# Kernel optimization log

Hardware: AMD Instinct MI355X
Metric: run time of the kernel (lower is better)

## Reference

```python
import jax, jax.numpy as jnp
import numpy as np

N_NODES = 50000
N_EDGES = 1_600_000
D_NODE = 64
D_EDGE = 16
HEADS = 4
ATT_F = 16  # features[0] / heads = 64 / 4
LN_EPS = 1e-6


def setup_inputs() -> dict:
    key = jax.random.key(0)
    ks = jax.random.split(key, 9)
    nodes = jax.random.normal(ks[0], (N_NODES, D_NODE), dtype=jnp.float32)
    edges = jax.random.normal(ks[1], (N_EDGES, D_EDGE), dtype=jnp.float32)
    receivers = jax.random.randint(ks[2], (N_EDGES,), 0, N_NODES)
    senders = jax.random.randint(ks[3], (N_EDGES,), 0, N_NODES)
    # he_normal-like scale for W (fan_in = input feature dim)
    W = jax.random.normal(ks[4], (HEADS, ATT_F, D_NODE), dtype=jnp.float32) * np.sqrt(2.0 / D_NODE)
    W_edge = jax.random.normal(ks[5], (HEADS, ATT_F, D_EDGE), dtype=jnp.float32) * np.sqrt(2.0 / D_EDGE)
    # xavier_normal-like scale for a
    a = jax.random.normal(ks[6], (HEADS, 3 * ATT_F), dtype=jnp.float32) * np.sqrt(2.0 / (HEADS + 3 * ATT_F))
    ln_scale = jnp.ones((HEADS * ATT_F,), dtype=jnp.float32)
    ln_bias = jnp.zeros((HEADS * ATT_F,), dtype=jnp.float32)
    return {"nodes": nodes, "edges": edges, "receivers": receivers, "senders": senders,
            "W": W, "W_edge": W_edge, "a": a, "ln_scale": ln_scale, "ln_bias": ln_bias}


def reference(nodes, edges, receivers, senders, W, W_edge, a, ln_scale, ln_bias):
    n = nodes.shape[0]
    # add self edges (zero edge features)
    self_idx = jnp.arange(n)
    r = jnp.concatenate([receivers, self_idx], axis=0)          # [Etot]
    s = jnp.concatenate([senders, self_idx], axis=0)            # [Etot]
    e = jnp.concatenate([edges, jnp.zeros((n, edges.shape[1]), edges.dtype)], axis=0)  # [Etot, De]

    # project node features once, then gather per edge
    Wn = jnp.einsum('hfi,ni->nhf', W, nodes)                    # [N, H, F]
    Ws = Wn[s]                                                   # [Etot, H, F]
    Wr = Wn[r]                                                   # [Etot, H, F]
    We = jnp.einsum('hfi,ei->ehf', W_edge, e)                   # [Etot, H, F]

    # attention logits: a . [Ws || Wr || We], computed without materializing the concat
    a_s, a_r, a_e = jnp.split(a, 3, axis=-1)                    # each [H, F]
    msg = (jnp.einsum('ehf,hf->eh', Ws, a_s)
           + jnp.einsum('ehf,hf->eh', Wr, a_r)
           + jnp.einsum('ehf,hf->eh', We, a_e))                 # [Etot, H]
    lm = jax.nn.leaky_relu(msg)

    # segment softmax over edges grouped by receiver
    seg_max = jax.ops.segment_max(lm, r, num_segments=n)        # [N, H]
    z = lm - seg_max[r]
    exp_z = jnp.exp(z)
    norm = jax.ops.segment_sum(exp_z, r, num_segments=n)        # [N, H]
    alpha = exp_z / norm[r]                                     # [Etot, H]

    # attention-weighted scatter-sum aggregation
    att_msg = alpha[:, :, None] * Ws                            # [Etot, H, F]
    aggr = jax.ops.segment_sum(att_msg, r, num_segments=n)      # [N, H, F]
    out = aggr.reshape(n, -1)                                   # [N, H*F]

    out = jax.nn.elu(out)
    # LayerNorm (flax default: eps=1e-6, scale & bias over last axis)
    mean = jnp.mean(out, axis=-1, keepdims=True)
    var = jnp.mean(jnp.square(out - mean), axis=-1, keepdims=True)
    out = (out - mean) * jax.lax.rsqrt(var + LN_EPS)
    out = out * ln_scale + ln_bias
    return out
```

## Files before the change

kernel.cpp:

```cpp
#include <hip/hip_runtime.h>
#include <hip/hip_fp16.h>

#define LEAKY_SLOPE 0.01f
#define LN_EPS 1e-6f
#define SUBS 8
#define CAP 352
#define MAXE (SUBS*CAP)
#define CSTRIDE 16

__device__ __forceinline__ float head_sel(int h, float a, float b, float c, float d) {
    float lo = (h & 1) ? b : a;
    float hi = (h & 1) ? d : c;
    return (h & 2) ? hi : lo;
}

__device__ __forceinline__ int xcc_id() {
    return (int)(__builtin_amdgcn_s_getreg(20 | (3 << 11)) & 7);
}

__global__ __launch_bounds__(256) void node_proj_kernel(
    const float* __restrict__ nodes, const float* __restrict__ W,
    const float* __restrict__ a, float* __restrict__ Wn,
    float* __restrict__ s_s, float* __restrict__ s_r,
    float* __restrict__ lm_self, int N)
{
    __shared__ float Wt[64][65];
    int t = threadIdx.x;
    #pragma unroll
    for (int k = 0; k < 16; k++) {
        int flat = k * 256 + t;
        Wt[flat & 63][flat >> 6] = W[flat];
    }
    __syncthreads();
    int lane = t & 63;
    int n = blockIdx.x * 4 + (t >> 6);
    if (n >= N) return;
    float nv = nodes[(size_t)n * 64 + lane];
    float acc = 0.f;
    #pragma unroll
    for (int i = 0; i < 64; i++)
        acc += Wt[i][lane] * __shfl(nv, i);
    Wn[(size_t)n * 64 + lane] = acc;
    int h = lane >> 4, f = lane & 15;
    float ps = acc * a[h * 48 + f];
    float pr = acc * a[h * 48 + 16 + f];
    #pragma unroll
    for (int off = 1; off < 16; off <<= 1) {
        ps += __shfl_xor(ps, off);
        pr += __shfl_xor(pr, off);
    }
    if (f == 0) {
        s_s[n * 4 + h] = ps;
        s_r[n * 4 + h] = pr;
        float v = ps + pr;
        lm_self[n * 4 + h] = v > 0.f ? v : LEAKY_SLOPE * v;
    }
}

__global__ __launch_bounds__(256) void edge_bin_kernel(
    const float* __restrict__ edges, const int* __restrict__ receivers,
    const int* __restrict__ senders, const float* __restrict__ W_edge,
    const float* __restrict__ a, const float* __restrict__ s_s,
    const float* __restrict__ s_r, int* __restrict__ cursor,
    int4* __restrict__ slab, int E)
{
    __shared__ float be[4][16];
    int t = threadIdx.x;
    int e = blockIdx.x * 256 + t;
    bool act = e < E;
    int r = 0, s = 0;
    if (act) { r = receivers[e]; s = senders[e]; }
    if (t < 64) {
        int h = t >> 4, i = t & 15;
        float sm = 0.f;
        #pragma unroll
        for (int f = 0; f < 16; f++)
            sm += W_edge[(h * 16 + f) * 16 + i] * a[h * 48 + 32 + f];
        be[h][i] = sm;
    }
    __syncthreads();
    if (!act) return;

    int b = r >> 6;
    int cidx = b * SUBS + xcc_id();
    int slot = atomicAdd(&cursor[cidx * CSTRIDE], 1);

    const float4* ef = (const float4*)(edges + (size_t)e * 16);
    float4 e0 = ef[0], e1 = ef[1], e2 = ef[2], e3 = ef[3];
    float4 ssv = ((const float4*)s_s)[s];
    float4 srv = ((const float4*)s_r)[r];
    float ev[16] = {e0.x, e0.y, e0.z, e0.w, e1.x, e1.y, e1.z, e1.w,
                    e2.x, e2.y, e2.z, e2.w, e3.x, e3.y, e3.z, e3.w};
    float ssa[4] = {ssv.x, ssv.y, ssv.z, ssv.w};
    float sra[4] = {srv.x, srv.y, srv.z, srv.w};
    float lm[4];
    #pragma unroll
    for (int hh = 0; hh < 4; hh++) {
        float se = 0.f;
        #pragma unroll
        for (int i = 0; i < 16; i++) se += be[hh][i] * ev[i];
        float v = ssa[hh] + sra[hh] + se;
        lm[hh] = v > 0.f ? v : LEAKY_SLOPE * v;
    }
    if (slot < CAP) {
        unsigned packA = (unsigned)__half_as_ushort(__float2half(lm[2])) |
                         ((unsigned)__half_as_ushort(__float2half(lm[3])) << 16);
        unsigned packB = (unsigned)s | ((unsigned)(r & 63) << 16);
        slab[(size_t)cidx * CAP + slot] =
            make_int4(__float_as_int(lm[0]), __float_as_int(lm[1]),
                      (int)packA, (int)packB);
    }
}

__global__ __launch_bounds__(256) void bucket_sort_kernel(
    const int* __restrict__ cursor, int4* __restrict__ slab,
    int2* __restrict__ meta, int N)
{
    __shared__ int4 raw[MAXE];
    __shared__ unsigned short perm[MAXE];
    __shared__ int cnt64[64];
    __shared__ int off64[64];
    __shared__ int cur64[64];

    int b = blockIdx.x;
    int t = threadIdx.x;
    int nn = min(64, N - b * 64);

    if (t < 64) cnt64[t] = 0;
    __syncthreads();

    int c[SUBS], basearr[SUBS];
    int tot = 0;
    #pragma unroll
    for (int sub = 0; sub < SUBS; sub++) {
        int cc = min(cursor[(b * SUBS + sub) * CSTRIDE], CAP);
        c[sub] = cc; basearr[sub] = tot; tot += cc;
    }

    #pragma unroll
    for (int sub = 0; sub < SUBS; sub++) {
        int cc = c[sub], bs = basearr[sub];
        const int4* src = slab + (size_t)(b * SUBS + sub) * CAP;
        for (int i = t; i < cc; i += 256) {
            int4 p = src[i];
            raw[bs + i] = p;
            atomicAdd(&cnt64[((unsigned)p.w >> 16) & 63], 1);
        }
    }
    __syncthreads();

    if (t < 64) {
        int v = cnt64[t];
        int incl = v;
        #pragma unroll
        for (int off = 1; off < 64; off <<= 1) {
            int u = __shfl_up(incl, off);
            if (t >= off) incl += u;
        }
        off64[t] = incl - v;
        cur64[t] = incl - v;
    }
    __syncthreads();

    for (int i = t; i < tot; i += 256) {
        int rl = ((unsigned)raw[i].w >> 16) & 63;
        int pos = atomicAdd(&cur64[rl], 1);
        perm[pos] = (unsigned short)i;
    }
    __syncthreads();

    int4* dst = slab + (size_t)b * MAXE;
    for (int pos = t; pos < tot; pos += 256)
        dst[pos] = raw[perm[pos]];

    if (t < nn)
        meta[b * 64 + t] = make_int2(b * MAXE + off64[t], cnt64[t]);
}

__global__ __launch_bounds__(256) void node_aggr_kernel(
    const float* __restrict__ Wn, const float* __restrict__ lm_self,
    const int2* __restrict__ meta, const int4* __restrict__ sorted,
    const float* __restrict__ ln_scale, const float* __restrict__ ln_bias,
    float* __restrict__ out, int N)
{
    __shared__ float lds_w[4][64][4];
    __shared__ int   lds_s[4][64];
    int t = threadIdx.x;
    int lane = t & 63;
    int wv = t >> 6;
    int n = blockIdx.x * 4 + wv;
    if (n >= N) return;
    int2 mt = meta[n];
    int beg = mt.x, cntn = mt.y;
    int h = lane >> 4;

    float acc = 0.f, acc2 = 0.f;
    float p0 = 0.f, p1 = 0.f, p2 = 0.f, p3 = 0.f;

    for (int base = 0; base < cntn; base += 64) {
        int j = base + lane;
        float w0 = 0.f, w1 = 0.f, w2 = 0.f, w3 = 0.f;
        int sv = 0;
        if (j < cntn) {
            int4 pl = sorted[beg + j];
            w0 = __expf(__int_as_float(pl.x));
            w1 = __expf(__int_as_float(pl.y));
            unsigned pa = (unsigned)pl.z;
            w2 = __expf(__half2float(__ushort_as_half((unsigned short)(pa & 0xFFFFu))));
            w3 = __expf(__half2float(__ushort_as_half((unsigned short)(pa >> 16))));
            sv = (int)((unsigned)pl.w & 0xFFFFu);
        }
        p0 += w0; p1 += w1; p2 += w2; p3 += w3;
        lds_s[wv][lane] = sv;
        *(float4*)&lds_w[wv][lane][0] = make_float4(w0, w1, w2, w3);
        int cnt = min(64, cntn - base);
        int k = 0;
        for (; k + 1 < cnt; k += 2) {
            int   sk0 = lds_s[wv][k];
            int   sk1 = lds_s[wv][k + 1];
            float a0  = lds_w[wv][k][h];
            float a1  = lds_w[wv][k + 1][h];
            acc  += a0 * Wn[(size_t)sk0 * 64 + lane];
            acc2 += a1 * Wn[(size_t)sk1 * 64 + lane];
        }
        if (k < cnt)
            acc += lds_w[wv][k][h] * Wn[(size_t)lds_s[wv][k] * 64 + lane];
    }
    acc += acc2;

    #pragma unroll
    for (int off = 1; off < 64; off <<= 1) {
        p0 += __shfl_xor(p0, off);
        p1 += __shfl_xor(p1, off);
        p2 += __shfl_xor(p2, off);
        p3 += __shfl_xor(p3, off);
    }
    float4 ls = ((const float4*)lm_self)[n];
    float ws0 = __expf(ls.x), ws1 = __expf(ls.y);
    float ws2 = __expf(ls.z), ws3 = __expf(ls.w);
    float totd  = head_sel(h, p0 + ws0, p1 + ws1, p2 + ws2, p3 + ws3);
    float wself = head_sel(h, ws0, ws1, ws2, ws3);
    acc = (acc + wself * Wn[(size_t)n * 64 + lane]) / totd;

    float y = acc > 0.f ? acc : expm1f(acc);
    float sum = y;
    #pragma unroll
    for (int off = 1; off < 64; off <<= 1) sum += __shfl_xor(sum, off);
    float mean = sum * 0.015625f;
    float d = y - mean;
    float vs = d * d;
    #pragma unroll
    for (int off = 1; off < 64; off <<= 1) vs += __shfl_xor(vs, off);
    float var = vs * 0.015625f;
    float o = d * rsqrtf(var + LN_EPS) * ln_scale[lane] + ln_bias[lane];
    out[(size_t)n * 64 + lane] = o;
}

extern "C" void kernel_launch(void* const* d_in, const int* in_sizes, int n_in,
                              void* d_out, int out_size, void* d_ws, size_t ws_size,
                              hipStream_t stream) {
    const float* nodes     = (const float*)d_in[0];
    const float* edges     = (const float*)d_in[1];
    const int*   receivers = (const int*)d_in[2];
    const int*   senders   = (const int*)d_in[3];
    const float* W         = (const float*)d_in[4];
    const float* W_edge    = (const float*)d_in[5];
    const float* a         = (const float*)d_in[6];
    const float* ln_scale  = (const float*)d_in[7];
    const float* ln_bias   = (const float*)d_in[8];
    float* out = (float*)d_out;

    int N = in_sizes[0] / 64;
    int E = in_sizes[2];
    int NB = (N + 63) / 64;

    char* ws = (char*)d_ws;
    size_t off = 0;
    auto alloc = [&](size_t bytes) -> void* {
        void* p = ws + off;
        off += (bytes + 15) & ~(size_t)15;
        return p;
    };
    float* Wn      = (float*)alloc((size_t)N * 64 * 4);
    float* s_s     = (float*)alloc((size_t)N * 4 * 4);
    float* s_r     = (float*)alloc((size_t)N * 4 * 4);
    float* lm_self = (float*)alloc((size_t)N * 4 * 4);
    int*   cursor  = (int*)alloc((size_t)NB * SUBS * CSTRIDE * 4);
    int2*  meta    = (int2*)alloc((size_t)N * 8);
    int4*  slab    = (int4*)alloc((size_t)NB * MAXE * 16);
    (void)ws_size; (void)n_in; (void)out_size;

    hipMemsetAsync(cursor, 0, (size_t)NB * SUBS * CSTRIDE * 4, stream);

    node_proj_kernel<<<(N + 3) / 4, 256, 0, stream>>>(
        nodes, W, a, Wn, s_s, s_r, lm_self, N);
    edge_bin_kernel<<<(E + 255) / 256, 256, 0, stream>>>(
        edges, receivers, senders, W_edge, a, s_s, s_r, cursor, slab, E);
    bucket_sort_kernel<<<NB, 256, 0, stream>>>(cursor, slab, meta, N);
    node_aggr_kernel<<<(N + 3) / 4, 256, 0, stream>>>(
        Wn, lm_self, meta, slab, ln_scale, ln_bias, out, N);
}
```

Before: 375.3 us.

## Fuse bucket sort with per-node aggregation and drop the sorted slab write-back

The separate bucket-sort and aggregation kernels are merged into one kernel per 64-node bucket. The sort now builds only an LDS permutation of slab indices, and each wave then aggregates 16 nodes by reading slab entries through that permutation. This removes the sorted-slab write-back, the meta array and one kernel launch. The cursor atomic is also relaxed to workgroup scope to make binning cheaper. The cost is far fewer waves (one block per bucket, each wave handling nodes serially), which may hurt latency hiding on the gathers; the workgroup-scope atomic on a cross-block counter is also semantically risky.

```diff
diff --git a/kernel.cpp b/kernel.cpp
--- a/kernel.cpp
+++ b/kernel.cpp
@@ -16,6 +16,13 @@
 
 __device__ __forceinline__ int xcc_id() {
     return (int)(__builtin_amdgcn_s_getreg(20 | (3 << 11)) & 7);
+}
+
+__device__ __forceinline__ float unpack_lm(int h, int4 p) {
+    unsigned pa = (unsigned)p.z;
+    float lm2 = __half2float(__ushort_as_half((unsigned short)(pa & 0xFFFFu)));
+    float lm3 = __half2float(__ushort_as_half((unsigned short)(pa >> 16)));
+    return head_sel(h, __int_as_float(p.x), __int_as_float(p.y), lm2, lm3);
 }
 
 __global__ __launch_bounds__(256) void node_proj_kernel(
@@ -83,7 +90,9 @@
 
     int b = r >> 6;
     int cidx = b * SUBS + xcc_id();
-    int slot = atomicAdd(&cursor[cidx * CSTRIDE], 1);
+    int slot = __hip_atomic_fetch_add(&cursor[cidx * CSTRIDE], 1,
+                                      __ATOMIC_RELAXED,
+                                      __HIP_MEMORY_SCOPE_WORKGROUP);
 
     const float4* ef = (const float4*)(edges + (size_t)e * 16);
     float4 e0 = ef[0], e1 = ef[1], e2 = ef[2], e3 = ef[3];
@@ -112,11 +121,13 @@
     }
 }
 
-__global__ __launch_bounds__(256) void bucket_sort_kernel(
-    const int* __restrict__ cursor, int4* __restrict__ slab,
-    int2* __restrict__ meta, int N)
+__global__ __launch_bounds__(256) void sort_aggr_kernel(
+    const float* __restrict__ Wn, const float* __restrict__ lm_self,
+    const int* __restrict__ cursor, const int4* __restrict__ slab,
+    const float* __restrict__ ln_scale, const float* __restrict__ ln_bias,
+    float* __restrict__ out, int N)
 {
-    __shared__ int4 raw[MAXE];
+    __shared__ unsigned tmp[MAXE];
     __shared__ unsigned short perm[MAXE];
     __shared__ int cnt64[64];
     __shared__ int off64[64];
@@ -124,7 +135,6 @@
 
     int b = blockIdx.x;
     int t = threadIdx.x;
-    int nn = min(64, N - b * 64);
 
     if (t < 64) cnt64[t] = 0;
     __syncthreads();
@@ -136,15 +146,17 @@
         int cc = min(cursor[(b * SUBS + sub) * CSTRIDE], CAP);
         c[sub] = cc; basearr[sub] = tot; tot += cc;
     }
+    const int4* slabB = slab + (size_t)b * MAXE;
 
     #pragma unroll
     for (int sub = 0; sub < SUBS; sub++) {
         int cc = c[sub], bs = basearr[sub];
-        const int4* src = slab + (size_t)(b * SUBS + sub) * CAP;
         for (int i = t; i < cc; i += 256) {
-            int4 p = src[i];
-            raw[bs + i] = p;
-            atomicAdd(&cnt64[((unsigned)p.w >> 16) & 63], 1);
+            int idx = sub * CAP + i;
+            int4 p = slabB[idx];
+            int rl = (int)(((unsigned)p.w >> 16) & 63u);
+            tmp[bs + i] = ((unsigned)idx << 6) | (unsigned)rl;
+            atomicAdd(&cnt64[rl], 1);
         }
     }
     __syncthreads();
@@ -163,97 +175,63 @@
     __syncthreads();
 
     for (int i = t; i < tot; i += 256) {
-        int rl = ((unsigned)raw[i].w >> 16) & 63;
+        unsigned u = tmp[i];
+        int rl = (int)(u & 63u);
         int pos = atomicAdd(&cur64[rl], 1);
-        perm[pos] = (unsigned short)i;
-    }
-    __syncthreads();
-
-    int4* dst = slab + (size_t)b * MAXE;
-    for (int pos = t; pos < tot; pos += 256)
-        dst[pos] = raw[perm[pos]];
-
-    if (t < nn)
-        meta[b * 64 + t] = make_int2(b * MAXE + off64[t], cnt64[t]);
-}
-
-__global__ __launch_bounds__(256) void node_aggr_kernel(
-    const float* __restrict__ Wn, const float* __restrict__ lm_self,
-    const int2* __restrict__ meta, const int4* __restrict__ sorted,
-    const float* __restrict__ ln_scale, const float* __restrict__ ln_bias,
-    float* __restrict__ out, int N)
-{
-    __shared__ float lds_w[4][64][4];
-    __shared__ int   lds_s[4][64];
-    int t = threadIdx.x;
+        perm[pos] = (unsigned short)(u >> 6);
+    }
+    __syncthreads();
+
     int lane = t & 63;
     int wv = t >> 6;
-    int n = blockIdx.x * 4 + wv;
-    if (n >= N) return;
-    int2 mt = meta[n];
-    int beg = mt.x, cntn = mt.y;
     int h = lane >> 4;
 
-    float acc = 0.f, acc2 = 0.f;
-    float p0 = 0.f, p1 = 0.f, p2 = 0.f, p3 = 0.f;
-
-    for (int base = 0; base < cntn; base += 64) {
-        int j = base + lane;
-        float w0 = 0.f, w1 = 0.f, w2 = 0.f, w3 = 0.f;
-        int sv = 0;
-        if (j < cntn) {
-            int4 pl = sorted[beg + j];
-            w0 = __expf(__int_as_float(pl.x));
-            w1 = __expf(__int_as_float(pl.y));
-            unsigned pa = (unsigned)pl.z;
-            w2 = __expf(__half2float(__ushort_as_half((unsigned short)(pa & 0xFFFFu))));
-            w3 = __expf(__half2float(__ushort_as_half((unsigned short)(pa >> 16))));
-            sv = (int)((unsigned)pl.w & 0xFFFFu);
-        }
-        p0 += w0; p1 += w1; p2 += w2; p3 += w3;
-        lds_s[wv][lane] = sv;
-        *(float4*)&lds_w[wv][lane][0] = make_float4(w0, w1, w2, w3);
-        int cnt = min(64, cntn - base);
-        int k = 0;
-        for (; k + 1 < cnt; k += 2) {
-            int   sk0 = lds_s[wv][k];
-            int   sk1 = lds_s[wv][k + 1];
-            float a0  = lds_w[wv][k][h];
-            float a1  = lds_w[wv][k + 1][h];
-            acc  += a0 * Wn[(size_t)sk0 * 64 + lane];
-            acc2 += a1 * Wn[(size_t)sk1 * 64 + lane];
-        }
-        if (k < cnt)
-            acc += lds_w[wv][k][h] * Wn[(size_t)lds_s[wv][k] * 64 + lane];
-    }
-    acc += acc2;
-
-    #pragma unroll
-    for (int off = 1; off < 64; off <<= 1) {
-        p0 += __shfl_xor(p0, off);
-        p1 += __shfl_xor(p1, off);
-        p2 += __shfl_xor(p2, off);
-        p3 += __shfl_xor(p3, off);
-    }
-    float4 ls = ((const float4*)lm_self)[n];
-    float ws0 = __expf(ls.x), ws1 = __expf(ls.y);
-    float ws2 = __expf(ls.z), ws3 = __expf(ls.w);
-    float totd  = head_sel(h, p0 + ws0, p1 + ws1, p2 + ws2, p3 + ws3);
-    float wself = head_sel(h, ws0, ws1, ws2, ws3);
-    acc = (acc + wself * Wn[(size_t)n * 64 + lane]) / totd;
-
-    float y = acc > 0.f ? acc : expm1f(acc);
-    float sum = y;
-    #pragma unroll
-    for (int off = 1; off < 64; off <<= 1) sum += __shfl_xor(sum, off);
-    float mean = sum * 0.015625f;
-    float d = y - mean;
-    float vs = d * d;
-    #pragma unroll
-    for (int off = 1; off < 64; off <<= 1) vs += __shfl_xor(vs, off);
-    float var = vs * 0.015625f;
-    float o = d * rsqrtf(var + LN_EPS) * ln_scale[lane] + ln_bias[lane];
-    out[(size_t)n * 64 + lane] = o;
+    for (int k = 0; k < 16; k++) {
+        int nloc = wv * 16 + k;
+        int n = b * 64 + nloc;
+        if (n >= N) break;
+        int cnt = cnt64[nloc];
+        int off = off64[nloc];
+        float acc = 0.f, acc2 = 0.f, den = 0.f, den2 = 0.f;
+        int j = 0;
+        for (; j + 1 < cnt; j += 2) {
+            int i0 = perm[off + j];
+            int i1 = perm[off + j + 1];
+            int4 p0 = slabB[i0];
+            int4 p1 = slabB[i1];
+            float w0 = __expf(unpack_lm(h, p0));
+            float w1 = __expf(unpack_lm(h, p1));
+            int s0 = (int)((unsigned)p0.w & 0xFFFFu);
+            int s1 = (int)((unsigned)p1.w & 0xFFFFu);
+            acc  += w0 * Wn[(size_t)s0 * 64 + lane]; den  += w0;
+            acc2 += w1 * Wn[(size_t)s1 * 64 + lane]; den2 += w1;
+        }
+        if (j < cnt) {
+            int i0 = perm[off + j];
+            int4 p0 = slabB[i0];
+            float w0 = __expf(unpack_lm(h, p0));
+            int s0 = (int)((unsigned)p0.w & 0xFFFFu);
+            acc += w0 * Wn[(size_t)s0 * 64 + lane]; den += w0;
+        }
+        acc += acc2; den += den2;
+
+        float4 ls = ((const float4*)lm_self)[n];
+        float wself = __expf(head_sel(h, ls.x, ls.y, ls.z, ls.w));
+        acc = (acc + wself * Wn[(size_t)n * 64 + lane]) / (den + wself);
+
+        float y = acc > 0.f ? acc : expm1f(acc);
+        float sum = y;
+        #pragma unroll
+        for (int o2 = 1; o2 < 64; o2 <<= 1) sum += __shfl_xor(sum, o2);
+        float mean = sum * 0.015625f;
+        float d = y - mean;
+        float vs = d * d;
+        #pragma unroll
+        for (int o2 = 1; o2 < 64; o2 <<= 1) vs += __shfl_xor(vs, o2);
+        float var = vs * 0.015625f;
+        float o = d * rsqrtf(var + LN_EPS) * ln_scale[lane] + ln_bias[lane];
+        out[(size_t)n * 64 + lane] = o;
+    }
 }
 
 extern "C" void kernel_launch(void* const* d_in, const int* in_sizes, int n_in,
@@ -286,7 +264,6 @@
     float* s_r     = (float*)alloc((size_t)N * 4 * 4);
     float* lm_self = (float*)alloc((size_t)N * 4 * 4);
     int*   cursor  = (int*)alloc((size_t)NB * SUBS * CSTRIDE * 4);
-    int2*  meta    = (int2*)alloc((size_t)N * 8);
     int4*  slab    = (int4*)alloc((size_t)NB * MAXE * 16);
     (void)ws_size; (void)n_in; (void)out_size;
 
@@ -296,7 +273,6 @@
         nodes, W, a, Wn, s_s, s_r, lm_self, N);
     edge_bin_kernel<<<(E + 255) / 256, 256, 0, stream>>>(
         edges, receivers, senders, W_edge, a, s_s, s_r, cursor, slab, E);
-    bucket_sort_kernel<<<NB, 256, 0, stream>>>(cursor, slab, meta, N);
-    node_aggr_kernel<<<(N + 3) / 4, 256, 0, stream>>>(
-        Wn, lm_self, meta, slab, ln_scale, ln_bias, out, N);
-}
+    sort_aggr_kernel<<<NB, 256, 0, stream>>>(
+        Wn, lm_self, cursor, slab, ln_scale, ln_bias, out, N);
+}
```

Result: slower. 430.9 us (+14.8%).

## Fold cursor memset into node projection, keep W in registers, relax atomic scope

Applied to the files above, without the earlier changes.

The separate memset of the bin cursors is removed; the node projection kernel now zeroes them, which saves one launch on the stream. The node projection is restructured: each lane holds its row of W in 64 registers, read as float4 loads, and each wave processes four nodes with vectorized node-row reads. This replaces the shared-memory transpose and shuffle broadcast. The edge binning atomic is changed to a relaxed, workgroup-scope fetch-add, relying on the per-XCC cursor split to keep it correct. That scope reduction is a correctness risk if the hardware does not place those atomics in a shared L2.

```diff
diff --git a/kernel.cpp b/kernel.cpp
--- a/kernel.cpp
+++ b/kernel.cpp
@@ -22,38 +22,51 @@
     const float* __restrict__ nodes, const float* __restrict__ W,
     const float* __restrict__ a, float* __restrict__ Wn,
     float* __restrict__ s_s, float* __restrict__ s_r,
-    float* __restrict__ lm_self, int N)
+    float* __restrict__ lm_self, int* __restrict__ cursor,
+    int ncursor, int N)
 {
-    __shared__ float Wt[64][65];
     int t = threadIdx.x;
-    #pragma unroll
-    for (int k = 0; k < 16; k++) {
-        int flat = k * 256 + t;
-        Wt[flat & 63][flat >> 6] = W[flat];
-    }
-    __syncthreads();
+    int ci = blockIdx.x * 256 + t;
+    if (ci < ncursor) cursor[ci] = 0;
+
     int lane = t & 63;
-    int n = blockIdx.x * 4 + (t >> 6);
-    if (n >= N) return;
-    float nv = nodes[(size_t)n * 64 + lane];
-    float acc = 0.f;
-    #pragma unroll
-    for (int i = 0; i < 64; i++)
-        acc += Wt[i][lane] * __shfl(nv, i);
-    Wn[(size_t)n * 64 + lane] = acc;
+    int wv = t >> 6;
+    float w[64];
+    const float4* W4 = (const float4*)W;
+    #pragma unroll
+    for (int i = 0; i < 16; i++) {
+        float4 v = W4[lane * 16 + i];
+        w[4*i] = v.x; w[4*i+1] = v.y; w[4*i+2] = v.z; w[4*i+3] = v.w;
+    }
     int h = lane >> 4, f = lane & 15;
-    float ps = acc * a[h * 48 + f];
-    float pr = acc * a[h * 48 + 16 + f];
-    #pragma unroll
-    for (int off = 1; off < 16; off <<= 1) {
-        ps += __shfl_xor(ps, off);
-        pr += __shfl_xor(pr, off);
-    }
-    if (f == 0) {
-        s_s[n * 4 + h] = ps;
-        s_r[n * 4 + h] = pr;
-        float v = ps + pr;
-        lm_self[n * 4 + h] = v > 0.f ? v : LEAKY_SLOPE * v;
+    float as_ = a[h * 48 + f];
+    float ar_ = a[h * 48 + 16 + f];
+    int n0 = blockIdx.x * 16 + wv * 4;
+    #pragma unroll
+    for (int k = 0; k < 4; k++) {
+        int n = n0 + k;
+        if (n >= N) break;
+        const float4* row4 = (const float4*)(nodes + (size_t)n * 64);
+        float acc = 0.f;
+        #pragma unroll
+        for (int c = 0; c < 16; c++) {
+            float4 v = row4[c];
+            acc += v.x * w[4*c] + v.y * w[4*c+1] + v.z * w[4*c+2] + v.w * w[4*c+3];
+        }
+        Wn[(size_t)n * 64 + lane] = acc;
+        float ps = acc * as_;
+        float pr = acc * ar_;
+        #pragma unroll
+        for (int off = 1; off < 16; off <<= 1) {
+            ps += __shfl_xor(ps, off);
+            pr += __shfl_xor(pr, off);
+        }
+        if (f == 0) {
+            s_s[n * 4 + h] = ps;
+            s_r[n * 4 + h] = pr;
+            float v = ps + pr;
+            lm_self[n * 4 + h] = v > 0.f ? v : LEAKY_SLOPE * v;
+        }
     }
 }
 
@@ -83,7 +96,9 @@
 
     int b = r >> 6;
     int cidx = b * SUBS + xcc_id();
-    int slot = atomicAdd(&cursor[cidx * CSTRIDE], 1);
+    int slot = __hip_atomic_fetch_add(&cursor[cidx * CSTRIDE], 1,
+                                      __ATOMIC_RELAXED,
+                                      __HIP_MEMORY_SCOPE_WORKGROUP);
 
     const float4* ef = (const float4*)(edges + (size_t)e * 16);
     float4 e0 = ef[0], e1 = ef[1], e2 = ef[2], e3 = ef[3];
@@ -273,6 +288,7 @@
     int N = in_sizes[0] / 64;
     int E = in_sizes[2];
     int NB = (N + 63) / 64;
+    int ncursor = NB * SUBS * CSTRIDE;
 
     char* ws = (char*)d_ws;
     size_t off = 0;
@@ -285,15 +301,13 @@
     float* s_s     = (float*)alloc((size_t)N * 4 * 4);
     float* s_r     = (float*)alloc((size_t)N * 4 * 4);
     float* lm_self = (float*)alloc((size_t)N * 4 * 4);
-    int*   cursor  = (int*)alloc((size_t)NB * SUBS * CSTRIDE * 4);
+    int*   cursor  = (int*)alloc((size_t)ncursor * 4);
     int2*  meta    = (int2*)alloc((size_t)N * 8);
     int4*  slab    = (int4*)alloc((size_t)NB * MAXE * 16);
     (void)ws_size; (void)n_in; (void)out_size;
 
-    hipMemsetAsync(cursor, 0, (size_t)NB * SUBS * CSTRIDE * 4, stream);
-
-    node_proj_kernel<<<(N + 3) / 4, 256, 0, stream>>>(
-        nodes, W, a, Wn, s_s, s_r, lm_self, N);
+    node_proj_kernel<<<(N + 15) / 16, 256, 0, stream>>>(
+        nodes, W, a, Wn, s_s, s_r, lm_self, cursor, ncursor, N);
     edge_bin_kernel<<<(E + 255) / 256, 256, 0, stream>>>(
         edges, receivers, senders, W_edge, a, s_s, s_r, cursor, slab, E);
     bucket_sort_kernel<<<NB, 256, 0, stream>>>(cursor, slab, meta, N);
```

After: 373.3 us. About the same (-0.5%).
